# Optimization experiments

Measured on AMD Instinct MI355X. Metric: run time of the kernel, lower is better.

The kernel has to match this reference:

```python
import jax, jax.numpy as jnp
import numpy as np

ITEM_NUM = 50000
TARGET_ITEM_NUM = 50000
EMB = 128
N_LAYERS = 3
N_EDGES = 800000
N_NODES = ITEM_NUM + 1  # forward uses item_emb[:item_num+1]


def gcn_conv(x, row, col, W, b, n):
    """PyG GCNConv: symmetric-normalized aggregation with self-loops.
    out = D^{-1/2} (A + I) D^{-1/2} (x @ W) + b
    """
    h = x @ W  # [n, d]
    loops = jnp.arange(n)
    r = jnp.concatenate([row, loops])  # source
    c = jnp.concatenate([col, loops])  # target
    deg = jax.ops.segment_sum(jnp.ones(r.shape[0], x.dtype), c, num_segments=n)
    dinv = jnp.where(deg > 0, deg ** -0.5, jnp.zeros_like(deg))
    norm = dinv[r] * dinv[c]  # [E+n]
    out = jax.ops.segment_sum(h[r] * norm[:, None], c, num_segments=n)
    return out + b


def setup_inputs() -> dict:
    key = jax.random.key(0)
    k0, k1, k2 = jax.random.split(key, 3)
    edge_index = jax.random.randint(k0, (2, N_EDGES), 0, N_NODES)
    total = ITEM_NUM + TARGET_ITEM_NUM + 1
    # xavier_uniform for embedding table and per-layer GCN weights
    lim_e = float(np.sqrt(6.0 / (total + EMB)))
    item_emb = jax.random.uniform(k1, (total, EMB), jnp.float32, -lim_e, lim_e)
    lim_w = float(np.sqrt(6.0 / (EMB + EMB)))
    W = jax.random.uniform(k2, (N_LAYERS, EMB, EMB), jnp.float32, -lim_w, lim_w)
    b = jnp.zeros((N_LAYERS, EMB), jnp.float32)
    return {"edge_index": edge_index, "item_emb": item_emb, "W": W, "b": b}


def reference(edge_index, item_emb, W, b):
    n = N_NODES
    row, col = edge_index[0], edge_index[1]
    embeds = [item_emb[:n]]
    for i in range(N_LAYERS):
        embeds.append(gcn_conv(embeds[-1], row, col, W[i], b[i], n))
    return sum(embeds)  # [n, EMB], sum over layer embeddings
```

## Files before the change

kernel.cpp:

```cpp
#include <hip/hip_runtime.h>
#include <hip/hip_bf16.h>


constexpr int NN   = 50001;
constexpr int D    = 128;
constexpr int NPAD = 50048;
constexpr int NBK  = 196;
constexpr int PB   = 784;
constexpr int PCAP = 7680;
constexpr int NQB  = NBK * 4;
constexpr int CAPQ = 2048;
constexpr int ZROW = NPAD - 1;

using bf16x8 = __attribute__((ext_vector_type(8))) short;
using f32x4  = __attribute__((ext_vector_type(4))) float;
using u16x8  = __attribute__((ext_vector_type(8))) unsigned short;
using u32x4  = __attribute__((ext_vector_type(4))) unsigned;

__device__ __forceinline__ ushort f2b(float f) {
    unsigned u = __float_as_uint(f);
    return (ushort)((u + 0x7FFFu + ((u >> 16) & 1u)) >> 16);
}
__device__ __forceinline__ float b2f(ushort u) {
    return __uint_as_float((unsigned)u << 16);
}

__global__ __launch_bounds__(256)
void k_build(const int* __restrict__ row, const int* __restrict__ col,
             int* __restrict__ partCur, unsigned* __restrict__ part,
             const float* __restrict__ W, ushort* __restrict__ Wt, int E) {
    int b = blockIdx.x, t = threadIdx.x;
    if (b < PB) {
        __shared__ int hist[256];
        __shared__ int base[256];
        hist[t] = 0;
        __syncthreads();
        int e0 = b * 1024;
        unsigned rec[4];
        int bkt[4];
#pragma unroll
        for (int k = 0; k < 4; k++) {
            int e = e0 + k * 256 + t;
            if (e < E) {
                int r = row[e], c = col[e];
                rec[k] = (unsigned)r | ((unsigned)(c & 255) << 16);
                bkt[k] = c >> 8;
                atomicAdd(&hist[bkt[k]], 1);
            } else bkt[k] = -1;
        }
        __syncthreads();
        if (hist[t] > 0) base[t] = t * PCAP + atomicAdd(&partCur[t], hist[t]);
        __syncthreads();
#pragma unroll
        for (int k = 0; k < 4; k++) {
            if (bkt[k] >= 0) {
                int pos = atomicAdd(&base[bkt[k]], 1);
                if (pos < (bkt[k] + 1) * PCAP) part[pos] = rec[k];
            }
        }
    } else {
        int idx = (b - PB) * 256 + t;
        int l = idx >> 14, rem = idx & 16383;
        int c = rem >> 7, k = rem & 127;
        Wt[idx] = f2b(W[l * D * D + k * D + c]);
    }
}

__global__ __launch_bounds__(256)
void k_scat(const unsigned* __restrict__ part, const int* __restrict__ partCur,
            float* __restrict__ dinv, unsigned* __restrict__ rp,
            ushort* __restrict__ meta, int n) {
    __shared__ int hist[64];
    __shared__ int sm[64];
    __shared__ int off[64];
    __shared__ int cur[64];
    int b = blockIdx.x, t = threadIdx.x;
    int B = b >> 2, q = b & 3;
    int node0 = B * 256 + q * 64;
    int T = min(partCur[B], PCAP);
    const unsigned* pb = part + (size_t)B * PCAP;
    if (t < 64) hist[t] = 0;
    __syncthreads();
    for (int i = t; i < T; i += 256) {
        int dl = (int)(pb[i] >> 16);
        if ((dl >> 6) == q) atomicAdd(&hist[dl & 63], 1);
    }
    __syncthreads();
    if (t < 64) sm[t] = (hist[t] + 15) & ~15;
    __syncthreads();
    for (int ofs = 1; ofs < 64; ofs <<= 1) {
        int u = 0;
        if (t >= ofs && t < 64) u = sm[t - ofs];
        __syncthreads();
        if (t < 64) sm[t] += u;
        __syncthreads();
    }
    if (t < 64) {
        int v = hist[t];
        off[t] = sm[t] - ((v + 15) & ~15);
        cur[t] = 0;
        int node = node0 + t;
        if (node < n) {
            dinv[node] = rsqrtf((float)v + 1.0f);
            rp[node] = (unsigned)(b * CAPQ + off[t]) | ((unsigned)v << 21);
        }
    }
    __syncthreads();
    for (int i = t; i < T; i += 256) {
        unsigned rec = pb[i];
        int dl = (int)(rec >> 16);
        if ((dl >> 6) == q) {
            int m = dl & 63;
            int pos = off[m] + atomicAdd(&cur[m], 1);
            if (pos < CAPQ) meta[(size_t)b * CAPQ + pos] = (ushort)(rec & 0xFFFFu);
        }
    }
    if (t < 64) {
        int v = hist[t], pv = (v + 15) & ~15;
        int base = off[t];
        for (int p = v; p < pv; p++)
            if (base + p < CAPQ) meta[(size_t)b * CAPQ + base + p] = (ushort)ZROW;
    }
}

constexpr int WT_LD = 136;
__global__ __launch_bounds__(256)
void k_gemm0(const float* __restrict__ emb, const ushort* __restrict__ WtL,
             const float* __restrict__ dinv, ushort* __restrict__ h, int n) {
    __shared__ ushort wlds[D * WT_LD];
    for (int idx = threadIdx.x; idx < D * (D / 8); idx += 256) {
        int r = idx >> 4, c8 = (idx & 15) * 8;
        *(uint4*)&wlds[r * WT_LD + c8] = *(const uint4*)&WtL[r * D + c8];
    }
    __syncthreads();

    int wave = threadIdx.x >> 6, lane = threadIdx.x & 63;
    int q = lane >> 4, i = lane & 15;
    int waveRow = blockIdx.x * 128 + wave * 32;

    bf16x8 a[2][4];
#pragma unroll
    for (int rt = 0; rt < 2; rt++) {
        const float* base = emb + (size_t)(waveRow + rt * 16 + i) * D + q * 8;
#pragma unroll
        for (int ks = 0; ks < 4; ks++) {
            float4 v0 = *(const float4*)(base + ks * 32);
            float4 v1 = *(const float4*)(base + ks * 32 + 4);
            bf16x8 aa;
            aa[0] = (short)f2b(v0.x); aa[1] = (short)f2b(v0.y);
            aa[2] = (short)f2b(v0.z); aa[3] = (short)f2b(v0.w);
            aa[4] = (short)f2b(v1.x); aa[5] = (short)f2b(v1.y);
            aa[6] = (short)f2b(v1.z); aa[7] = (short)f2b(v1.w);
            a[rt][ks] = aa;
        }
    }

    f32x4 acc[2][8] = {};
#pragma unroll
    for (int ct = 0; ct < 8; ct++) {
        const ushort* wbase = &wlds[(ct * 16 + i) * WT_LD + q * 8];
#pragma unroll
        for (int ks = 0; ks < 4; ks++) {
            bf16x8 bfr = *(const bf16x8*)(wbase + ks * 32);
            acc[0][ct] = __builtin_amdgcn_mfma_f32_16x16x32_bf16(a[0][ks], bfr, acc[0][ct], 0, 0, 0);
            acc[1][ct] = __builtin_amdgcn_mfma_f32_16x16x32_bf16(a[1][ks], bfr, acc[1][ct], 0, 0, 0);
        }
    }

#pragma unroll
    for (int rt = 0; rt < 2; rt++)
#pragma unroll
        for (int r4 = 0; r4 < 4; r4++) {
            int row = waveRow + rt * 16 + q * 4 + r4;
            float dv = (row < n) ? dinv[row] : 0.f;
#pragma unroll
            for (int ct = 0; ct < 8; ct++)
                h[(size_t)row * D + ct * 16 + i] = f2b(acc[rt][ct][r4] * dv);
        }
}

__global__ __launch_bounds__(256)
void k_fused(const unsigned* __restrict__ rp, const ushort* __restrict__ meta,
             const ushort* __restrict__ h_in,
             const float* __restrict__ dinv, const float* __restrict__ bias,
             const ushort* __restrict__ Wn,
             ushort* __restrict__ xb_out, ushort* __restrict__ h_out, int n) {
    __shared__ ushort xlds[16 * WT_LD];
    __shared__ float  sdinv[16];
    int tid  = threadIdx.x;
    int nl   = tid >> 4;
    int l    = tid & 15;
    int node0 = blockIdx.x * 16;
    int node  = node0 + nl;

    u16x8 w = {0, 0, 0, 0, 0, 0, 0, 0};
    float di = 0.f;
    if (node < n) {
        unsigned pk = rp[node];
        int s   = (int)(pk & 0x1FFFFFu);
        int deg = (int)(pk >> 21);
        const ushort* hl = h_in + (l << 3);

        u32x4 sv = *(const u32x4*)(hl + (size_t)node * D);
        di = dinv[node];
        const float4* bp = (const float4*)(bias + (l << 3));
        float4 b0 = bp[0], b1 = bp[1];

        float accL[4], accH[4];
#pragma unroll
        for (int k = 0; k < 4; k++) {
            accL[k] = __uint_as_float(sv[k] << 16);
            accH[k] = __uint_as_float(sv[k] & 0xFFFF0000u);
        }
        for (int j = 0; j < deg; j += 16) {
            u16x8 m0 = *(const u16x8*)&meta[s + j];
            u16x8 m1 = *(const u16x8*)&meta[s + j + 8];
            u32x4 v[16];
#pragma unroll
            for (int u = 0; u < 8; u++) v[u]     = *(const u32x4*)(hl + (size_t)m0[u] * D);
#pragma unroll
            for (int u = 0; u < 8; u++) v[8 + u] = *(const u32x4*)(hl + (size_t)m1[u] * D);
#pragma unroll
            for (int u = 0; u < 16; u++)
#pragma unroll
                for (int k = 0; k < 4; k++) {
                    accL[k] += __uint_as_float(v[u][k] << 16);
                    accH[k] += __uint_as_float(v[u][k] & 0xFFFF0000u);
                }
        }
        w[0] = f2b(fmaf(accL[0], di, b0.x));
        w[1] = f2b(fmaf(accH[0], di, b0.y));
        w[2] = f2b(fmaf(accL[1], di, b0.z));
        w[3] = f2b(fmaf(accH[1], di, b0.w));
        w[4] = f2b(fmaf(accL[2], di, b1.x));
        w[5] = f2b(fmaf(accH[2], di, b1.y));
        w[6] = f2b(fmaf(accL[3], di, b1.z));
        w[7] = f2b(fmaf(accH[3], di, b1.w));
        *(u16x8*)(xb_out + (size_t)node * D + (l << 3)) = w;
    }
    *(u16x8*)&xlds[nl * WT_LD + l * 8] = w;
    if (l == 0) sdinv[nl] = di;
    __syncthreads();

    int wave = tid >> 6, lane = tid & 63;
    int q = lane >> 4, i = lane & 15;

    bf16x8 a[4];
#pragma unroll
    for (int ks = 0; ks < 4; ks++)
        a[ks] = *(const bf16x8*)&xlds[i * WT_LD + ks * 32 + q * 8];

    f32x4 acc[2] = {};
#pragma unroll
    for (int ct = 0; ct < 2; ct++) {
        const ushort* wbase = &Wn[(size_t)(wave * 32 + ct * 16 + i) * D + q * 8];
#pragma unroll
        for (int ks = 0; ks < 4; ks++) {
            bf16x8 bfr = *(const bf16x8*)(wbase + ks * 32);
            acc[ct] = __builtin_amdgcn_mfma_f32_16x16x32_bf16(a[ks], bfr, acc[ct], 0, 0, 0);
        }
    }

#pragma unroll
    for (int r4 = 0; r4 < 4; r4++) {
        int rr = q * 4 + r4;
        float dv = sdinv[rr];
#pragma unroll
        for (int ct = 0; ct < 2; ct++)
            h_out[(size_t)(node0 + rr) * D + wave * 32 + ct * 16 + i] =
                f2b(acc[ct][r4] * dv);
    }
}

__global__ __launch_bounds__(256)
void k_pull_final(const unsigned* __restrict__ rp, const ushort* __restrict__ meta,
                  const ushort* __restrict__ h,
                  const float* __restrict__ dinv, const float* __restrict__ bias,
                  const float* __restrict__ emb, const ushort* __restrict__ x1,
                  const ushort* __restrict__ x2, float* __restrict__ out, int n) {
    int node = blockIdx.x * 16 + (threadIdx.x >> 4);
    int l    = threadIdx.x & 15;
    if (node >= n) return;
    unsigned pk = rp[node];
    int s   = (int)(pk & 0x1FFFFFu);
    int deg = (int)(pk >> 21);
    size_t o = (size_t)node * D + (l << 3);
    const ushort* hl = h + (l << 3);

    u32x4 sv = *(const u32x4*)(hl + (size_t)node * D);
    float di = dinv[node];
    const float4* bp = (const float4*)(bias + (l << 3));
    float4 b0 = bp[0], b1 = bp[1];
    const float4* ep = (const float4*)(emb + o);
    float4 e0 = ep[0], e1 = ep[1];
    u16x8 w1 = *(const u16x8*)(x1 + o);
    u16x8 w2 = *(const u16x8*)(x2 + o);

    float accL[4], accH[4];
#pragma unroll
    for (int k = 0; k < 4; k++) {
        accL[k] = __uint_as_float(sv[k] << 16);
        accH[k] = __uint_as_float(sv[k] & 0xFFFF0000u);
    }
    for (int j = 0; j < deg; j += 16) {
        u16x8 m0 = *(const u16x8*)&meta[s + j];
        u16x8 m1 = *(const u16x8*)&meta[s + j + 8];
        u32x4 v[16];
#pragma unroll
        for (int u = 0; u < 8; u++) v[u]     = *(const u32x4*)(hl + (size_t)m0[u] * D);
#pragma unroll
        for (int u = 0; u < 8; u++) v[8 + u] = *(const u32x4*)(hl + (size_t)m1[u] * D);
#pragma unroll
        for (int u = 0; u < 16; u++)
#pragma unroll
            for (int k = 0; k < 4; k++) {
                accL[k] += __uint_as_float(v[u][k] << 16);
                accH[k] += __uint_as_float(v[u][k] & 0xFFFF0000u);
            }
    }
    f32x4 o0, o1;
    o0[0] = e0.x + b2f(w1[0]) + b2f(w2[0]) + fmaf(accL[0], di, b0.x);
    o0[1] = e0.y + b2f(w1[1]) + b2f(w2[1]) + fmaf(accH[0], di, b0.y);
    o0[2] = e0.z + b2f(w1[2]) + b2f(w2[2]) + fmaf(accL[1], di, b0.z);
    o0[3] = e0.w + b2f(w1[3]) + b2f(w2[3]) + fmaf(accH[1], di, b0.w);
    o1[0] = e1.x + b2f(w1[4]) + b2f(w2[4]) + fmaf(accL[2], di, b1.x);
    o1[1] = e1.y + b2f(w1[5]) + b2f(w2[5]) + fmaf(accH[2], di, b1.y);
    o1[2] = e1.z + b2f(w1[6]) + b2f(w2[6]) + fmaf(accL[3], di, b1.z);
    o1[3] = e1.w + b2f(w1[7]) + b2f(w2[7]) + fmaf(accH[3], di, b1.w);
    __builtin_nontemporal_store(o0, (f32x4*)(out + o));
    __builtin_nontemporal_store(o1, (f32x4*)(out + o) + 1);
}

extern "C" void kernel_launch(void* const* d_in, const int* in_sizes, int n_in,
                              void* d_out, int out_size, void* d_ws, size_t ws_size,
                              hipStream_t stream) {
    const int*   edge = (const int*)d_in[0];
    const float* emb  = (const float*)d_in[1];
    const float* W    = (const float*)d_in[2];
    const float* b    = (const float*)d_in[3];
    float* out = (float*)d_out;

    const int E = in_sizes[0] / 2;
    const int n = NN;
    const int* row = edge;
    const int* col = edge + E;

    char* ws = (char*)d_ws;
    size_t off = 0;
    auto carve = [&](size_t bytes) { char* p = ws + off; off = (off + bytes + 511) / 512 * 512; return p; };
    int*      partCur = (int*)     carve(256 * 4);
    unsigned* part    = (unsigned*)carve((size_t)NBK * PCAP * 4);
    ushort*   meta    = (ushort*)  carve((size_t)NQB * CAPQ * 2);
    unsigned* rp      = (unsigned*)carve((size_t)n * 4);
    float*    dinv    = (float*)   carve((size_t)n * 4);
    ushort*   Wt      = (ushort*)  carve((size_t)3 * D * D * 2);
    ushort*   xb1     = (ushort*)  carve((size_t)NPAD * D * 2);
    ushort*   xb2     = (ushort*)  carve((size_t)NPAD * D * 2);
    ushort*   hA      = (ushort*)  carve((size_t)NPAD * D * 2);
    ushort*   hB      = (ushort*)  carve((size_t)NPAD * D * 2);

    (void)hipMemsetAsync(partCur, 0, 256 * 4, stream);

    const int build_blocks = PB + 192;
    k_build<<<build_blocks, 256, 0, stream>>>(row, col, partCur, part, W, Wt, E);
    k_scat <<<NQB, 256, 0, stream>>>(part, partCur, dinv, rp, meta, n);

    const int gemm_blocks  = NPAD / 128;
    const int fused_blocks = NPAD / 16;
    const int final_blocks = (n + 15) / 16;

    k_gemm0<<<gemm_blocks, 256, 0, stream>>>(emb, Wt, dinv, hA, n);
    k_fused<<<fused_blocks, 256, 0, stream>>>(rp, meta, hA, dinv, b,
                                              Wt + (size_t)1 * D * D, xb1, hB, n);
    k_fused<<<fused_blocks, 256, 0, stream>>>(rp, meta, hB, dinv, b + D,
                                              Wt + (size_t)2 * D * D, xb2, hA, n);
    k_pull_final<<<final_blocks, 256, 0, stream>>>(rp, meta, hA, dinv, b + 2 * D,
                                                   emb, xb1, xb2, out, n);
}
```

Before: 250.7 us.

## Replace bucketed partition CSR build with global-atomic degree count and scatter

Replaces the two-pass bucket-partition CSR construction (per-256-node partitions, then per-64-node local sort) with a classic three-kernel build: a global atomic degree histogram, a per-block scan that gets its base offset from a global cursor atomic, and an atomic-cursor scatter of source ids into a single meta array. This removes fixed per-bucket capacities and the staged partition buffer, at the cost of many global atomics on random destinations and an extra kernel launch. The neighbor order within each row becomes nondeterministic, and rows are no longer placed in node order because the cursor atomic hands out block bases in arbitrary order.

```diff
diff --git a/kernel.cpp b/kernel.cpp
--- a/kernel.cpp
+++ b/kernel.cpp
@@ -5,12 +5,8 @@
 constexpr int NN   = 50001;
 constexpr int D    = 128;
 constexpr int NPAD = 50048;
-constexpr int NBK  = 196;
-constexpr int PB   = 784;
-constexpr int PCAP = 7680;
-constexpr int NQB  = NBK * 4;
-constexpr int CAPQ = 2048;
 constexpr int ZROW = NPAD - 1;
+constexpr int METACAP = 1 << 21;
 
 using bf16x8 = __attribute__((ext_vector_type(8))) short;
 using f32x4  = __attribute__((ext_vector_type(4))) float;
@@ -26,40 +22,15 @@
 }
 
 __global__ __launch_bounds__(256)
-void k_build(const int* __restrict__ row, const int* __restrict__ col,
-             int* __restrict__ partCur, unsigned* __restrict__ part,
-             const float* __restrict__ W, ushort* __restrict__ Wt, int E) {
+void k_pre1(const int* __restrict__ col, int* __restrict__ deg,
+            const float* __restrict__ W, ushort* __restrict__ Wt, int E) {
+    int cb = (E + 255) >> 8;
     int b = blockIdx.x, t = threadIdx.x;
-    if (b < PB) {
-        __shared__ int hist[256];
-        __shared__ int base[256];
-        hist[t] = 0;
-        __syncthreads();
-        int e0 = b * 1024;
-        unsigned rec[4];
-        int bkt[4];
-#pragma unroll
-        for (int k = 0; k < 4; k++) {
-            int e = e0 + k * 256 + t;
-            if (e < E) {
-                int r = row[e], c = col[e];
-                rec[k] = (unsigned)r | ((unsigned)(c & 255) << 16);
-                bkt[k] = c >> 8;
-                atomicAdd(&hist[bkt[k]], 1);
-            } else bkt[k] = -1;
-        }
-        __syncthreads();
-        if (hist[t] > 0) base[t] = t * PCAP + atomicAdd(&partCur[t], hist[t]);
-        __syncthreads();
-#pragma unroll
-        for (int k = 0; k < 4; k++) {
-            if (bkt[k] >= 0) {
-                int pos = atomicAdd(&base[bkt[k]], 1);
-                if (pos < (bkt[k] + 1) * PCAP) part[pos] = rec[k];
-            }
-        }
+    if (b < cb) {
+        int e = b * 256 + t;
+        if (e < E) atomicAdd(&deg[col[e]], 1);
     } else {
-        int idx = (b - PB) * 256 + t;
+        int idx = (b - cb) * 256 + t;
         int l = idx >> 14, rem = idx & 16383;
         int c = rem >> 7, k = rem & 127;
         Wt[idx] = f2b(W[l * D * D + k * D + c]);
@@ -67,60 +38,42 @@
 }
 
 __global__ __launch_bounds__(256)
-void k_scat(const unsigned* __restrict__ part, const int* __restrict__ partCur,
+void k_pre2(const int* __restrict__ deg, unsigned* __restrict__ cursor,
             float* __restrict__ dinv, unsigned* __restrict__ rp,
             ushort* __restrict__ meta, int n) {
-    __shared__ int hist[64];
-    __shared__ int sm[64];
-    __shared__ int off[64];
-    __shared__ int cur[64];
-    int b = blockIdx.x, t = threadIdx.x;
-    int B = b >> 2, q = b & 3;
-    int node0 = B * 256 + q * 64;
-    int T = min(partCur[B], PCAP);
-    const unsigned* pb = part + (size_t)B * PCAP;
-    if (t < 64) hist[t] = 0;
+    __shared__ int sm[256];
+    __shared__ int sbase;
+    int t = threadIdx.x;
+    int node = blockIdx.x * 256 + t;
+    int v  = (node < n) ? deg[node] : 0;
+    int pv = (v + 15) & ~15;
+    sm[t] = pv;
     __syncthreads();
-    for (int i = t; i < T; i += 256) {
-        int dl = (int)(pb[i] >> 16);
-        if ((dl >> 6) == q) atomicAdd(&hist[dl & 63], 1);
-    }
+    for (int ofs = 1; ofs < 256; ofs <<= 1) {
+        int u = (t >= ofs) ? sm[t - ofs] : 0;
+        __syncthreads();
+        sm[t] += u;
+        __syncthreads();
+    }
+    if (t == 255) sbase = (int)atomicAdd(cursor, (unsigned)sm[255]);
     __syncthreads();
-    if (t < 64) sm[t] = (hist[t] + 15) & ~15;
-    __syncthreads();
-    for (int ofs = 1; ofs < 64; ofs <<= 1) {
-        int u = 0;
-        if (t >= ofs && t < 64) u = sm[t - ofs];
-        __syncthreads();
-        if (t < 64) sm[t] += u;
-        __syncthreads();
-    }
-    if (t < 64) {
-        int v = hist[t];
-        off[t] = sm[t] - ((v + 15) & ~15);
-        cur[t] = 0;
-        int node = node0 + t;
-        if (node < n) {
-            dinv[node] = rsqrtf((float)v + 1.0f);
-            rp[node] = (unsigned)(b * CAPQ + off[t]) | ((unsigned)v << 21);
-        }
-    }
-    __syncthreads();
-    for (int i = t; i < T; i += 256) {
-        unsigned rec = pb[i];
-        int dl = (int)(rec >> 16);
-        if ((dl >> 6) == q) {
-            int m = dl & 63;
-            int pos = off[m] + atomicAdd(&cur[m], 1);
-            if (pos < CAPQ) meta[(size_t)b * CAPQ + pos] = (ushort)(rec & 0xFFFFu);
-        }
-    }
-    if (t < 64) {
-        int v = hist[t], pv = (v + 15) & ~15;
-        int base = off[t];
-        for (int p = v; p < pv; p++)
-            if (base + p < CAPQ) meta[(size_t)b * CAPQ + base + p] = (ushort)ZROW;
-    }
+    int start = sbase + sm[t] - pv;
+    if (node < n) {
+        dinv[node] = rsqrtf((float)v + 1.0f);
+        rp[node] = (unsigned)start | ((unsigned)v << 21);
+        for (int p = v; p < pv; p++) meta[start + p] = (ushort)ZROW;
+    }
+}
+
+__global__ __launch_bounds__(256)
+void k_pre3(const int* __restrict__ row, const int* __restrict__ col,
+            const unsigned* __restrict__ rp, int* __restrict__ cur,
+            ushort* __restrict__ meta, int E) {
+    int e = blockIdx.x * 256 + threadIdx.x;
+    if (e >= E) return;
+    int src = row[e], dst = col[e];
+    int pos = (int)(rp[dst] & 0x1FFFFFu) + atomicAdd(&cur[dst], 1);
+    meta[pos] = (ushort)src;
 }
 
 constexpr int WT_LD = 136;
@@ -348,22 +301,26 @@
     char* ws = (char*)d_ws;
     size_t off = 0;
     auto carve = [&](size_t bytes) { char* p = ws + off; off = (off + bytes + 511) / 512 * 512; return p; };
-    int*      partCur = (int*)     carve(256 * 4);
-    unsigned* part    = (unsigned*)carve((size_t)NBK * PCAP * 4);
-    ushort*   meta    = (ushort*)  carve((size_t)NQB * CAPQ * 2);
-    unsigned* rp      = (unsigned*)carve((size_t)n * 4);
-    float*    dinv    = (float*)   carve((size_t)n * 4);
-    ushort*   Wt      = (ushort*)  carve((size_t)3 * D * D * 2);
-    ushort*   xb1     = (ushort*)  carve((size_t)NPAD * D * 2);
-    ushort*   xb2     = (ushort*)  carve((size_t)NPAD * D * 2);
-    ushort*   hA      = (ushort*)  carve((size_t)NPAD * D * 2);
-    ushort*   hB      = (ushort*)  carve((size_t)NPAD * D * 2);
-
-    (void)hipMemsetAsync(partCur, 0, 256 * 4, stream);
-
-    const int build_blocks = PB + 192;
-    k_build<<<build_blocks, 256, 0, stream>>>(row, col, partCur, part, W, Wt, E);
-    k_scat <<<NQB, 256, 0, stream>>>(part, partCur, dinv, rp, meta, n);
+    size_t z0 = off;
+    unsigned* cursor = (unsigned*)carve(512);
+    int*      cur    = (int*)     carve((size_t)n * 4);
+    int*      deg    = (int*)     carve((size_t)n * 4);
+    size_t zlen = off - z0;
+    unsigned* rp     = (unsigned*)carve((size_t)n * 4);
+    float*    dinv   = (float*)   carve((size_t)n * 4);
+    ushort*   Wt     = (ushort*)  carve((size_t)3 * D * D * 2);
+    ushort*   meta   = (ushort*)  carve((size_t)METACAP * 2);
+    ushort*   xb1    = (ushort*)  carve((size_t)NPAD * D * 2);
+    ushort*   xb2    = (ushort*)  carve((size_t)NPAD * D * 2);
+    ushort*   hA     = (ushort*)  carve((size_t)NPAD * D * 2);
+    ushort*   hB     = (ushort*)  carve((size_t)NPAD * D * 2);
+
+    (void)hipMemsetAsync(ws + z0, 0, zlen, stream);
+
+    const int cb = (E + 255) / 256;
+    k_pre1<<<cb + 192, 256, 0, stream>>>(col, deg, W, Wt, E);
+    k_pre2<<<(n + 255) / 256, 256, 0, stream>>>(deg, cursor, dinv, rp, meta, n);
+    k_pre3<<<cb, 256, 0, stream>>>(row, col, rp, cur, meta, E);
 
     const int gemm_blocks  = NPAD / 128;
     const int fused_blocks = NPAD / 16;
```

Result: slower. 297.5 us (+18.7%).
